# Performance work log

Measured on AMD Instinct MI355X. Metric: run time of the kernel, lower is better.

The kernel has to match this reference:

```python
import jax, jax.numpy as jnp
from jax import lax
import numpy as np


def setup_inputs() -> dict:
    key = jax.random.key(0)
    k1, k2 = jax.random.split(key)
    inputs = jax.random.normal(k1, (32, 64, 64, 128), dtype=jnp.float32)
    # glorot-like scale for a 3x3x128->256 kernel
    kernel = jax.random.normal(k2, (3, 3, 128, 256), dtype=jnp.float32) * 0.03
    return {"inputs": inputs, "kernel": kernel}


def reference(inputs, kernel):
    # Stride-1 VALID conv, NHWC inputs, HWIO kernel (same math as the unrolled
    # per-pixel patch*kernel + reduce_sum loop in conv2d_manual).
    conv = lax.conv_general_dilated(
        inputs, kernel,
        window_strides=(1, 1), padding="VALID",
        dimension_numbers=("NHWC", "HWIO", "NHWC"),
    )  # [B, OH, OW, F]
    B, OH, OW, F = conv.shape
    # Faithfully replicate the original TensorArray stack (OH*OW, B, F)
    # followed by a raw reshape to (B, OH, OW, F) (element-permuting).
    stacked = jnp.moveaxis(conv, 0, 2)            # (OH, OW, B, F)
    out = stacked.reshape(B, OH, OW, F)           # raw reshape, as in original
    return jax.nn.relu(out)
```

## Files before the change

kernel.cpp:

```cpp
#include <hip/hip_runtime.h>

typedef short bf16x8 __attribute__((ext_vector_type(8)));
typedef float f32x4 __attribute__((ext_vector_type(4)));
typedef unsigned short u16;

__device__ __forceinline__ u16 f2bf(float f) {
    unsigned u = __builtin_bit_cast(unsigned, f);
    u += 0x7FFF + ((u >> 16) & 1);
    return (u16)(u >> 16);
}

constexpr int Hh = 64, Ww = 64, Ci = 128;
constexpr int Fo = 256, OH = 62, OW = 62;
constexpr int Ktot = 3 * 3 * Ci;
constexpr int BM = 128, BK = 64;
constexpr int NSTEP = Ktot / BK;
constexpr int NWG = 1922;
constexpr long NEL_IN = 32L * 64 * 64 * 128;
constexpr size_t WS_IN_BYTES = (size_t)NEL_IN * 2;
constexpr size_t WS_WT_OFF   = WS_IN_BYTES;
constexpr size_t WS_NEED     = WS_IN_BYTES + 294912ull * 2;

#define GLD_LDS(src, dst) __builtin_amdgcn_global_load_lds( \
    (const __attribute__((address_space(1))) unsigned int*)(src), \
    (__attribute__((address_space(3))) unsigned int*)(dst), 16, 0, 0)

__global__ __launch_bounds__(256) void cvt_input(const float* __restrict__ in,
                                                 u16* __restrict__ ob) {
    const int i = blockIdx.x * 256 + threadIdx.x;
    const float4* s = (const float4*)in + (long)i * 2;
    float4 v0 = s[0], v1 = s[1];
    bf16x8 p;
    p[0] = (short)f2bf(v0.x); p[1] = (short)f2bf(v0.y);
    p[2] = (short)f2bf(v0.z); p[3] = (short)f2bf(v0.w);
    p[4] = (short)f2bf(v1.x); p[5] = (short)f2bf(v1.y);
    p[6] = (short)f2bf(v1.z); p[7] = (short)f2bf(v1.w);
    ((bf16x8*)ob)[i] = p;
}

__global__ __launch_bounds__(256) void cvt_wt(const float* __restrict__ wt,
                                              u16* __restrict__ ob) {
    const int t = blockIdx.x * 256 + threadIdx.x;
    const int f = t / 144, k8 = t % 144;
    bf16x8 p;
    #pragma unroll
    for (int j = 0; j < 8; ++j)
        p[j] = (short)f2bf(wt[(k8 * 8 + j) * Fo + f]);
    ((bf16x8*)ob)[f * 144 + k8] = p;
}

__global__ __launch_bounds__(256) void conv_mfma(
    const u16* __restrict__ inb,
    const u16* __restrict__ wtb,
    float* __restrict__ out)
{
    __shared__ __align__(16) short As0[BM * BK];
    __shared__ __align__(16) short Bs0[BM * BK];
    __shared__ __align__(16) short As1[BM * BK];
    __shared__ __align__(16) short Bs1[BM * BK];

    const int tid  = threadIdx.x;
    const int lane = tid & 63;
    const int wv   = tid >> 6;
    const int wr   = wv >> 1, wc = wv & 1;

    constexpr int q = NWG / 8, rr = NWG % 8;
    const int orig = blockIdx.x;
    const int xcd = orig & 7, idx = orig >> 3;
    const int wgid = (xcd < rr ? xcd * (q + 1) : rr * (q + 1) + (xcd - rr) * q) + idx;

    const int colb = wgid & 1;
    const int rowb = wgid >> 1;
    const int r0   = rowb * BM;
    const int f0g  = colb * 128;

    const int lrow8 = lane >> 3;
    const int schunk = ((lane & 7) ^ lrow8) * 16;
    long abyte[4], bbyte[4];
    #pragma unroll
    for (int j = 0; j < 4; ++j) {
        const int r  = r0 + wv * 32 + j * 8 + lrow8;
        const int bb = r & 31;
        const int pix = r >> 5;
        const int ow = pix % OW, oh = pix / OW;
        abyte[j] = (long)(((bb * Hh + oh) * Ww + ow) * Ci) * 2 + schunk;
        const int f = f0g + wv * 32 + j * 8 + lrow8;
        bbyte[j] = (long)f * (Ktot * 2) + schunk;
    }

    auto stage = [&](int step, short (&Asb)[BM * BK], short (&Bsb)[BM * BK]) {
        const int kb = step >> 1, c0 = (step & 1) << 6;
        const int kh = kb / 3, kw = kb % 3;
        const long tap = (long)((kh * Ww + kw) * Ci + c0) * 2;
        const long bof = (long)step * 128;
        #pragma unroll
        for (int j = 0; j < 4; ++j)
            GLD_LDS((const char*)inb + abyte[j] + tap, &Asb[(wv * 32 + j * 8) * BK]);
        #pragma unroll
        for (int j = 0; j < 4; ++j)
            GLD_LDS((const char*)wtb + bbyte[j] + bof, &Bsb[(wv * 32 + j * 8) * BK]);
    };

    f32x4 acc[4][4];
    #pragma unroll
    for (int m = 0; m < 4; ++m)
        #pragma unroll
        for (int n = 0; n < 4; ++n) acc[m][n] = (f32x4){0.f, 0.f, 0.f, 0.f};

    const int lrow = lane & 15;
    const int lq   = lane >> 4;

    auto compute = [&](const short (&Asb)[BM * BK], const short (&Bsb)[BM * BK]) {
        #pragma unroll
        for (int ks = 0; ks < 2; ++ks) {
            bf16x8 a[4], b[4];
            const int off = ks * 64 + lq * 16;
            #pragma unroll
            for (int m = 0; m < 4; ++m) {
                const int row = wr * 64 + m * 16 + lrow;
                a[m] = *(const bf16x8*)((const char*)&Asb[0] + row * 128 + (off ^ ((row & 7) << 4)));
            }
            #pragma unroll
            for (int n = 0; n < 4; ++n) {
                const int row = wc * 64 + n * 16 + lrow;
                b[n] = *(const bf16x8*)((const char*)&Bsb[0] + row * 128 + (off ^ ((row & 7) << 4)));
            }
            #pragma unroll
            for (int m = 0; m < 4; ++m)
                #pragma unroll
                for (int n = 0; n < 4; ++n)
                    acc[m][n] = __builtin_amdgcn_mfma_f32_16x16x32_bf16(a[m], b[n], acc[m][n], 0, 0, 0);
        }
    };

    stage(0, As0, Bs0);
    __syncthreads();

    for (int t = 0; t < NSTEP; t += 2) {
        stage(t + 1, As1, Bs1);
        compute(As0, Bs0);
        __syncthreads();
        if (t + 2 < NSTEP) stage(t + 2, As0, Bs0);
        compute(As1, Bs1);
        __syncthreads();
    }

    const int lcol = lane & 15;
    const int lr4  = (lane >> 4) * 4;
    #pragma unroll
    for (int m = 0; m < 4; ++m) {
        #pragma unroll
        for (int n = 0; n < 4; ++n) {
            const int col = f0g + wc * 64 + n * 16 + lcol;
            const int rowbase = r0 + wr * 64 + m * 16 + lr4;
            #pragma unroll
            for (int e = 0; e < 4; ++e) {
                float v = acc[m][n][e];
                out[(long)(rowbase + e) * Fo + col] = v > 0.f ? v : 0.f;
            }
        }
    }
}

__global__ __launch_bounds__(256) void conv_mfma_fb(
    const float* __restrict__ in, const float* __restrict__ wt,
    float* __restrict__ out)
{
    __shared__ __align__(16) short As[BM * BK];
    __shared__ __align__(16) short Bs[BM * BK];
    const int tid  = threadIdx.x;
    const int lane = tid & 63;
    const int wv   = tid >> 6;
    const int wr   = wv >> 1, wc = wv & 1;
    constexpr int q2 = NWG / 8, rr2 = NWG % 8;
    const int orig = blockIdx.x;
    const int xcd = orig & 7, idx = orig >> 3;
    const int wgid = (xcd < rr2 ? xcd * (q2 + 1) : rr2 * (q2 + 1) + (xcd - rr2) * q2) + idx;
    const int colb = wgid & 1;
    const int rowb = wgid >> 1;
    const int r0   = rowb * 128;
    const int f0g  = colb * 128;
    const int ai = tid >> 1;
    const int ah = tid & 1;
    const int r  = r0 + ai;
    const int bb  = r & 31;
    const int pix = r >> 5;
    const int ow  = pix % OW;
    const int oh  = pix / OW;
    const float* abase = in + ((bb * Hh + oh) * Ww + ow) * Ci;
    const int bk = tid & 63;
    const int bf = (tid >> 6) * 32;

    auto loadA = [&](int step, float4 (&pa)[8]) {
        const int kb = step >> 1;
        const int c0 = (step & 1) << 6;
        const int kh = kb / 3, kw = kb % 3;
        const float* src = abase + (kh * Ww + kw) * Ci + c0 + ah * 32;
        #pragma unroll
        for (int c = 0; c < 8; ++c) pa[c] = ((const float4*)src)[c];
    };
    auto writeA = [&](const float4 (&pa)[8]) {
        char* dst = (char*)As + ai * 128;
        const int swz = (ai & 7) << 4;
        #pragma unroll
        for (int c = 0; c < 4; ++c) {
            float4 v0 = pa[2 * c], v1 = pa[2 * c + 1];
            bf16x8 pk;
            pk[0] = (short)f2bf(v0.x); pk[1] = (short)f2bf(v0.y);
            pk[2] = (short)f2bf(v0.z); pk[3] = (short)f2bf(v0.w);
            pk[4] = (short)f2bf(v1.x); pk[5] = (short)f2bf(v1.y);
            pk[6] = (short)f2bf(v1.z); pk[7] = (short)f2bf(v1.w);
            *(bf16x8*)(dst + ((ah * 64 + c * 16) ^ swz)) = pk;
        }
    };
    auto loadB = [&](int step, float4 (&pb)[8]) {
        const float* src = wt + (step * BK + bk) * Fo + f0g + bf;
        #pragma unroll
        for (int c = 0; c < 8; ++c) pb[c] = ((const float4*)src)[c];
    };
    auto writeB = [&](const float4 (&pb)[8]) {
        const int k2 = bk * 2;
        #pragma unroll
        for (int c = 0; c < 8; ++c) {
            float4 v = pb[c];
            const int fl = bf + c * 4;
            *(u16*)((char*)Bs + (fl + 0) * 128 + (k2 ^ (((fl + 0) & 7) << 4))) = f2bf(v.x);
            *(u16*)((char*)Bs + (fl + 1) * 128 + (k2 ^ (((fl + 1) & 7) << 4))) = f2bf(v.y);
            *(u16*)((char*)Bs + (fl + 2) * 128 + (k2 ^ (((fl + 2) & 7) << 4))) = f2bf(v.z);
            *(u16*)((char*)Bs + (fl + 3) * 128 + (k2 ^ (((fl + 3) & 7) << 4))) = f2bf(v.w);
        }
    };

    f32x4 acc[4][4];
    #pragma unroll
    for (int m = 0; m < 4; ++m)
        #pragma unroll
        for (int n = 0; n < 4; ++n) acc[m][n] = (f32x4){0.f, 0.f, 0.f, 0.f};
    {
        float4 pa[8], pb[8];
        loadA(0, pa); loadB(0, pb);
        writeA(pa); writeB(pb);
    }
    __syncthreads();
    const int lrow = lane & 15;
    const int lq   = lane >> 4;
    for (int step = 0; step < NSTEP; ++step) {
        float4 na[8], nb[8];
        if (step + 1 < NSTEP) { loadA(step + 1, na); loadB(step + 1, nb); }
        #pragma unroll
        for (int ks = 0; ks < 2; ++ks) {
            bf16x8 a[4], b[4];
            const int off = ks * 64 + lq * 16;
            #pragma unroll
            for (int m = 0; m < 4; ++m) {
                const int row = wr * 64 + m * 16 + lrow;
                a[m] = *(const bf16x8*)((const char*)As + row * 128 + (off ^ ((row & 7) << 4)));
            }
            #pragma unroll
            for (int n = 0; n < 4; ++n) {
                const int row = wc * 64 + n * 16 + lrow;
                b[n] = *(const bf16x8*)((const char*)Bs + row * 128 + (off ^ ((row & 7) << 4)));
            }
            #pragma unroll
            for (int m = 0; m < 4; ++m)
                #pragma unroll
                for (int n = 0; n < 4; ++n)
                    acc[m][n] = __builtin_amdgcn_mfma_f32_16x16x32_bf16(a[m], b[n], acc[m][n], 0, 0, 0);
        }
        __syncthreads();
        if (step + 1 < NSTEP) { writeA(na); writeB(nb); }
        __syncthreads();
    }
    const int lcol = lane & 15;
    const int lr4  = (lane >> 4) * 4;
    #pragma unroll
    for (int m = 0; m < 4; ++m) {
        #pragma unroll
        for (int n = 0; n < 4; ++n) {
            const int col = f0g + wc * 64 + n * 16 + lcol;
            const int rowbase = r0 + wr * 64 + m * 16 + lr4;
            #pragma unroll
            for (int e = 0; e < 4; ++e) {
                float v = acc[m][n][e];
                out[(rowbase + e) * Fo + col] = v > 0.f ? v : 0.f;
            }
        }
    }
}

extern "C" void kernel_launch(void* const* d_in, const int* in_sizes, int n_in,
                              void* d_out, int out_size, void* d_ws, size_t ws_size,
                              hipStream_t stream) {
    const float* in  = (const float*)d_in[0];
    const float* wt  = (const float*)d_in[1];
    float* out = (float*)d_out;
    if (ws_size >= WS_NEED) {
        u16* inb = (u16*)d_ws;
        u16* wtb = (u16*)((char*)d_ws + WS_WT_OFF);
        cvt_input<<<dim3(8192), dim3(256), 0, stream>>>(in, inb);
        cvt_wt<<<dim3(144), dim3(256), 0, stream>>>(wt, wtb);
        conv_mfma<<<dim3(NWG), dim3(256), 0, stream>>>(inb, wtb, out);
    } else {
        conv_mfma_fb<<<dim3(NWG), dim3(256), 0, stream>>>(in, wt, out);
    }
}
```

Before: 107.0 us.

## Enlarge conv tile to 256x256 with 8 waves and deeper prefetch

The MFMA conv kernel now gives each workgroup a 256-row by all-256-filter output tile with 512 threads (8 waves, each computing 128x64), so 481 workgroups replace 1922. Loads are issued two stages ahead, and synchronisation uses explicit vmcnt waits with raw barriers, with setprio raised around the MFMA bursts. The aim is more reuse per LDS load, fewer redundant input reads, and overlap of global-to-LDS copies with compute. The costs are higher register pressure from 32 accumulators per wave, lower occupancy, a tail workgroup that needs row clamping and guarded stores, and uneven load across the 256 CUs with only 481 groups.

```diff
diff --git a/kernel.cpp b/kernel.cpp
--- a/kernel.cpp
+++ b/kernel.cpp
@@ -13,9 +13,10 @@
 constexpr int Hh = 64, Ww = 64, Ci = 128;
 constexpr int Fo = 256, OH = 62, OW = 62;
 constexpr int Ktot = 3 * 3 * Ci;
-constexpr int BM = 128, BK = 64;
+constexpr int M_TOT = 123008;
+constexpr int BM = 256, BK = 64;
 constexpr int NSTEP = Ktot / BK;
-constexpr int NWG = 1922;
+constexpr int NWG = 481;
 constexpr long NEL_IN = 32L * 64 * 64 * 128;
 constexpr size_t WS_IN_BYTES = (size_t)NEL_IN * 2;
 constexpr size_t WS_WT_OFF   = WS_IN_BYTES;
@@ -24,6 +25,7 @@
 #define GLD_LDS(src, dst) __builtin_amdgcn_global_load_lds( \
     (const __attribute__((address_space(1))) unsigned int*)(src), \
     (__attribute__((address_space(3))) unsigned int*)(dst), 16, 0, 0)
+#define MEMFENCE asm volatile("" ::: "memory")
 
 __global__ __launch_bounds__(256) void cvt_input(const float* __restrict__ in,
                                                  u16* __restrict__ ob) {
@@ -49,7 +51,7 @@
     ((bf16x8*)ob)[f * 144 + k8] = p;
 }
 
-__global__ __launch_bounds__(256) void conv_mfma(
+__global__ __launch_bounds__(512) void conv_mfma(
     const u16* __restrict__ inb,
     const u16* __restrict__ wtb,
     float* __restrict__ out)
@@ -62,29 +64,26 @@
     const int tid  = threadIdx.x;
     const int lane = tid & 63;
     const int wv   = tid >> 6;
-    const int wr   = wv >> 1, wc = wv & 1;
+    const int wr   = wv >> 2, wc = wv & 3;
 
     constexpr int q = NWG / 8, rr = NWG % 8;
     const int orig = blockIdx.x;
     const int xcd = orig & 7, idx = orig >> 3;
     const int wgid = (xcd < rr ? xcd * (q + 1) : rr * (q + 1) + (xcd - rr) * q) + idx;
-
-    const int colb = wgid & 1;
-    const int rowb = wgid >> 1;
-    const int r0   = rowb * BM;
-    const int f0g  = colb * 128;
+    const int r0 = wgid * BM;
 
     const int lrow8 = lane >> 3;
     const int schunk = ((lane & 7) ^ lrow8) * 16;
     long abyte[4], bbyte[4];
     #pragma unroll
     for (int j = 0; j < 4; ++j) {
-        const int r  = r0 + wv * 32 + j * 8 + lrow8;
+        int r = r0 + wv * 32 + j * 8 + lrow8;
+        r = r < M_TOT ? r : M_TOT - 1;
         const int bb = r & 31;
         const int pix = r >> 5;
         const int ow = pix % OW, oh = pix / OW;
         abyte[j] = (long)(((bb * Hh + oh) * Ww + ow) * Ci) * 2 + schunk;
-        const int f = f0g + wv * 32 + j * 8 + lrow8;
+        const int f = wv * 32 + j * 8 + lrow8;
         bbyte[j] = (long)f * (Ktot * 2) + schunk;
     }
 
@@ -101,9 +100,9 @@
             GLD_LDS((const char*)wtb + bbyte[j] + bof, &Bsb[(wv * 32 + j * 8) * BK]);
     };
 
-    f32x4 acc[4][4];
-    #pragma unroll
-    for (int m = 0; m < 4; ++m)
+    f32x4 acc[8][4];
+    #pragma unroll
+    for (int m = 0; m < 8; ++m)
         #pragma unroll
         for (int n = 0; n < 4; ++n) acc[m][n] = (f32x4){0.f, 0.f, 0.f, 0.f};
 
@@ -113,50 +112,91 @@
     auto compute = [&](const short (&Asb)[BM * BK], const short (&Bsb)[BM * BK]) {
         #pragma unroll
         for (int ks = 0; ks < 2; ++ks) {
-            bf16x8 a[4], b[4];
+            bf16x8 a[8], b[4];
             const int off = ks * 64 + lq * 16;
             #pragma unroll
-            for (int m = 0; m < 4; ++m) {
-                const int row = wr * 64 + m * 16 + lrow;
+            for (int m = 0; m < 8; ++m) {
+                const int row = wr * 128 + m * 16 + lrow;
                 a[m] = *(const bf16x8*)((const char*)&Asb[0] + row * 128 + (off ^ ((row & 7) << 4)));
             }
             #pragma unroll
             for (int n = 0; n < 4; ++n) {
-                const int row = wc * 64 + n * 16 + lrow;
-                b[n] = *(const bf16x8*)((const char*)&Bsb[0] + row * 128 + (off ^ ((row & 7) << 4)));
-            }
-            #pragma unroll
-            for (int m = 0; m < 4; ++m)
+                const int frow = wc * 64 + n * 16 + lrow;
+                b[n] = *(const bf16x8*)((const char*)&Bsb[0] + frow * 128 + (off ^ ((frow & 7) << 4)));
+            }
+            __builtin_amdgcn_s_setprio(1);
+            #pragma unroll
+            for (int m = 0; m < 8; ++m)
                 #pragma unroll
                 for (int n = 0; n < 4; ++n)
                     acc[m][n] = __builtin_amdgcn_mfma_f32_16x16x32_bf16(a[m], b[n], acc[m][n], 0, 0, 0);
+            __builtin_amdgcn_s_setprio(0);
         }
     };
 
     stage(0, As0, Bs0);
-    __syncthreads();
+    stage(1, As1, Bs1);
+    asm volatile("s_waitcnt vmcnt(8)" ::: "memory");
+    __builtin_amdgcn_s_barrier();
+    MEMFENCE;
 
     for (int t = 0; t < NSTEP; t += 2) {
-        stage(t + 1, As1, Bs1);
         compute(As0, Bs0);
-        __syncthreads();
-        if (t + 2 < NSTEP) stage(t + 2, As0, Bs0);
+        MEMFENCE;
+        __builtin_amdgcn_s_barrier();
+        MEMFENCE;
+        if (t + 2 < NSTEP) {
+            stage(t + 2, As0, Bs0);
+            asm volatile("s_waitcnt vmcnt(8)" ::: "memory");
+        } else {
+            asm volatile("s_waitcnt vmcnt(0)" ::: "memory");
+        }
+        __builtin_amdgcn_s_barrier();
+        MEMFENCE;
+
         compute(As1, Bs1);
-        __syncthreads();
+        MEMFENCE;
+        __builtin_amdgcn_s_barrier();
+        MEMFENCE;
+        if (t + 3 < NSTEP) {
+            stage(t + 3, As1, Bs1);
+            asm volatile("s_waitcnt vmcnt(8)" ::: "memory");
+        } else {
+            asm volatile("s_waitcnt vmcnt(0)" ::: "memory");
+        }
+        __builtin_amdgcn_s_barrier();
+        MEMFENCE;
     }
 
     const int lcol = lane & 15;
     const int lr4  = (lane >> 4) * 4;
-    #pragma unroll
-    for (int m = 0; m < 4; ++m) {
-        #pragma unroll
-        for (int n = 0; n < 4; ++n) {
-            const int col = f0g + wc * 64 + n * 16 + lcol;
-            const int rowbase = r0 + wr * 64 + m * 16 + lr4;
-            #pragma unroll
-            for (int e = 0; e < 4; ++e) {
-                float v = acc[m][n][e];
-                out[(long)(rowbase + e) * Fo + col] = v > 0.f ? v : 0.f;
+    const int col  = wc * 64 + lcol;
+    if (r0 + BM <= M_TOT) {
+        #pragma unroll
+        for (int m = 0; m < 8; ++m) {
+            const int rowbase = r0 + wr * 128 + m * 16 + lr4;
+            #pragma unroll
+            for (int n = 0; n < 4; ++n) {
+                #pragma unroll
+                for (int e = 0; e < 4; ++e) {
+                    float v = acc[m][n][e];
+                    out[(long)(rowbase + e) * Fo + col + n * 16] = v > 0.f ? v : 0.f;
+                }
+            }
+        }
+    } else {
+        #pragma unroll
+        for (int m = 0; m < 8; ++m) {
+            const int rowbase = r0 + wr * 128 + m * 16 + lr4;
+            #pragma unroll
+            for (int n = 0; n < 4; ++n) {
+                #pragma unroll
+                for (int e = 0; e < 4; ++e) {
+                    if (rowbase + e < M_TOT) {
+                        float v = acc[m][n][e];
+                        out[(long)(rowbase + e) * Fo + col + n * 16] = v > 0.f ? v : 0.f;
+                    }
+                }
             }
         }
     }
@@ -166,13 +206,15 @@
     const float* __restrict__ in, const float* __restrict__ wt,
     float* __restrict__ out)
 {
-    __shared__ __align__(16) short As[BM * BK];
-    __shared__ __align__(16) short Bs[BM * BK];
+    constexpr int FBM = 128;
+    __shared__ __align__(16) short As[FBM * BK];
+    __shared__ __align__(16) short Bs[FBM * BK];
     const int tid  = threadIdx.x;
     const int lane = tid & 63;
     const int wv   = tid >> 6;
     const int wr   = wv >> 1, wc = wv & 1;
-    constexpr int q2 = NWG / 8, rr2 = NWG % 8;
+    constexpr int NWG_FB = 1922;
+    constexpr int q2 = NWG_FB / 8, rr2 = NWG_FB % 8;
     const int orig = blockIdx.x;
     const int xcd = orig & 7, idx = orig >> 3;
     const int wgid = (xcd < rr2 ? xcd * (q2 + 1) : rr2 * (q2 + 1) + (xcd - rr2) * q2) + idx;
@@ -227,7 +269,7 @@
             *(u16*)((char*)Bs + (fl + 0) * 128 + (k2 ^ (((fl + 0) & 7) << 4))) = f2bf(v.x);
             *(u16*)((char*)Bs + (fl + 1) * 128 + (k2 ^ (((fl + 1) & 7) << 4))) = f2bf(v.y);
             *(u16*)((char*)Bs + (fl + 2) * 128 + (k2 ^ (((fl + 2) & 7) << 4))) = f2bf(v.z);
-            *(u16*)((char*)Bs + (fl + 3) * 128 + (k2 ^ (((fl + 3) & 7) << 4))) = f2bf(v.w);
+            *(u16*)((char*)Bs + (fl + 3) * 128 + (k2 ^ (((fl + 3) << 4) & 0x70))) = f2bf(v.w);
         }
     };
 
@@ -299,8 +341,8 @@
         u16* wtb = (u16*)((char*)d_ws + WS_WT_OFF);
         cvt_input<<<dim3(8192), dim3(256), 0, stream>>>(in, inb);
         cvt_wt<<<dim3(144), dim3(256), 0, stream>>>(wt, wtb);
-        conv_mfma<<<dim3(NWG), dim3(256), 0, stream>>>(inb, wtb, out);
+        conv_mfma<<<dim3(NWG), dim3(512), 0, stream>>>(inb, wtb, out);
     } else {
-        conv_mfma_fb<<<dim3(NWG), dim3(256), 0, stream>>>(in, wt, out);
-    }
-}
+        conv_mfma_fb<<<dim3(1922), dim3(256), 0, stream>>>(in, wt, out);
+    }
+}
```

After: 107.0 us. No clear change (+0.0%).

## Load weight fragments directly from global into registers, dropping B LDS staging

Applied to the files above, without the earlier changes.

Weights are pre-permuted at conversion time into an MFMA-fragment-ordered layout, so each lane can read its B operands straight from global memory into registers, double-buffered across steps. The B shared-memory buffers and their LDS reads are removed, halving LDS use and LDS traffic. The cost is more VGPRs for two sets of eight bf16x8 fragments and direct global loads that depend on L2 hits for the shared weight tile, which may lower occupancy or expose load latency.

```diff
diff --git a/kernel.cpp b/kernel.cpp
--- a/kernel.cpp
+++ b/kernel.cpp
@@ -41,12 +41,14 @@
 __global__ __launch_bounds__(256) void cvt_wt(const float* __restrict__ wt,
                                               u16* __restrict__ ob) {
     const int t = blockIdx.x * 256 + threadIdx.x;
-    const int f = t / 144, k8 = t % 144;
+    const int lq  = t & 3;
+    const int f   = (t >> 2) & 255;
+    const int sks = t >> 10;
     bf16x8 p;
     #pragma unroll
     for (int j = 0; j < 8; ++j)
-        p[j] = (short)f2bf(wt[(k8 * 8 + j) * Fo + f]);
-    ((bf16x8*)ob)[f * 144 + k8] = p;
+        p[j] = (short)f2bf(wt[(sks * 32 + lq * 8 + j) * Fo + f]);
+    ((bf16x8*)ob)[t] = p;
 }
 
 __global__ __launch_bounds__(256) void conv_mfma(
@@ -55,9 +57,7 @@
     float* __restrict__ out)
 {
     __shared__ __align__(16) short As0[BM * BK];
-    __shared__ __align__(16) short Bs0[BM * BK];
     __shared__ __align__(16) short As1[BM * BK];
-    __shared__ __align__(16) short Bs1[BM * BK];
 
     const int tid  = threadIdx.x;
     const int lane = tid & 63;
@@ -72,11 +72,10 @@
     const int colb = wgid & 1;
     const int rowb = wgid >> 1;
     const int r0   = rowb * BM;
-    const int f0g  = colb * 128;
 
     const int lrow8 = lane >> 3;
     const int schunk = ((lane & 7) ^ lrow8) * 16;
-    long abyte[4], bbyte[4];
+    long abyte[4];
     #pragma unroll
     for (int j = 0; j < 4; ++j) {
         const int r  = r0 + wv * 32 + j * 8 + lrow8;
@@ -84,36 +83,40 @@
         const int pix = r >> 5;
         const int ow = pix % OW, oh = pix / OW;
         abyte[j] = (long)(((bb * Hh + oh) * Ww + ow) * Ci) * 2 + schunk;
-        const int f = f0g + wv * 32 + j * 8 + lrow8;
-        bbyte[j] = (long)f * (Ktot * 2) + schunk;
-    }
-
-    auto stage = [&](int step, short (&Asb)[BM * BK], short (&Bsb)[BM * BK]) {
+    }
+
+    auto stage = [&](int step, short (&Asb)[BM * BK]) {
         const int kb = step >> 1, c0 = (step & 1) << 6;
         const int kh = kb / 3, kw = kb % 3;
         const long tap = (long)((kh * Ww + kw) * Ci + c0) * 2;
-        const long bof = (long)step * 128;
         #pragma unroll
         for (int j = 0; j < 4; ++j)
             GLD_LDS((const char*)inb + abyte[j] + tap, &Asb[(wv * 32 + j * 8) * BK]);
-        #pragma unroll
-        for (int j = 0; j < 4; ++j)
-            GLD_LDS((const char*)wtb + bbyte[j] + bof, &Bsb[(wv * 32 + j * 8) * BK]);
-    };
-
-    f32x4 acc[4][4];
-    #pragma unroll
-    for (int m = 0; m < 4; ++m)
-        #pragma unroll
-        for (int n = 0; n < 4; ++n) acc[m][n] = (f32x4){0.f, 0.f, 0.f, 0.f};
+    };
 
     const int lrow = lane & 15;
     const int lq   = lane >> 4;
 
-    auto compute = [&](const short (&Asb)[BM * BK], const short (&Bsb)[BM * BK]) {
+    const bf16x8* bsrc = (const bf16x8*)wtb;
+    const int bbase = (colb * 128 + wc * 64 + lrow) * 4 + lq;
+    auto loadB = [&](int step, bf16x8 (&bf)[8]) {
+        #pragma unroll
+        for (int ks = 0; ks < 2; ++ks)
+            #pragma unroll
+            for (int n = 0; n < 4; ++n)
+                bf[ks * 4 + n] = bsrc[(step * 2 + ks) * 1024 + bbase + n * 64];
+    };
+
+    f32x4 acc[4][4];
+    #pragma unroll
+    for (int m = 0; m < 4; ++m)
+        #pragma unroll
+        for (int n = 0; n < 4; ++n) acc[m][n] = (f32x4){0.f, 0.f, 0.f, 0.f};
+
+    auto compute = [&](const short (&Asb)[BM * BK], const bf16x8 (&bfr)[8]) {
         #pragma unroll
         for (int ks = 0; ks < 2; ++ks) {
-            bf16x8 a[4], b[4];
+            bf16x8 a[4];
             const int off = ks * 64 + lq * 16;
             #pragma unroll
             for (int m = 0; m < 4; ++m) {
@@ -121,27 +124,29 @@
                 a[m] = *(const bf16x8*)((const char*)&Asb[0] + row * 128 + (off ^ ((row & 7) << 4)));
             }
             #pragma unroll
-            for (int n = 0; n < 4; ++n) {
-                const int row = wc * 64 + n * 16 + lrow;
-                b[n] = *(const bf16x8*)((const char*)&Bsb[0] + row * 128 + (off ^ ((row & 7) << 4)));
-            }
-            #pragma unroll
             for (int m = 0; m < 4; ++m)
                 #pragma unroll
                 for (int n = 0; n < 4; ++n)
-                    acc[m][n] = __builtin_amdgcn_mfma_f32_16x16x32_bf16(a[m], b[n], acc[m][n], 0, 0, 0);
-        }
-    };
-
-    stage(0, As0, Bs0);
+                    acc[m][n] = __builtin_amdgcn_mfma_f32_16x16x32_bf16(a[m], bfr[ks * 4 + n], acc[m][n], 0, 0, 0);
+        }
+    };
+
+    bf16x8 b0[8], b1[8];
+
+    stage(0, As0);
+    loadB(0, b0);
     __syncthreads();
 
     for (int t = 0; t < NSTEP; t += 2) {
-        stage(t + 1, As1, Bs1);
-        compute(As0, Bs0);
+        stage(t + 1, As1);
+        loadB(t + 1, b1);
+        compute(As0, b0);
         __syncthreads();
-        if (t + 2 < NSTEP) stage(t + 2, As0, Bs0);
-        compute(As1, Bs1);
+        if (t + 2 < NSTEP) {
+            stage(t + 2, As0);
+            loadB(t + 2, b0);
+        }
+        compute(As1, b1);
         __syncthreads();
     }
 
@@ -151,7 +156,7 @@
     for (int m = 0; m < 4; ++m) {
         #pragma unroll
         for (int n = 0; n < 4; ++n) {
-            const int col = f0g + wc * 64 + n * 16 + lcol;
+            const int col = colb * 128 + wc * 64 + n * 16 + lcol;
             const int rowbase = r0 + wr * 64 + m * 16 + lr4;
             #pragma unroll
             for (int e = 0; e < 4; ++e) {
```

Measured after the change: 132.5 us. 23.9% more time.

## Widen K tile to a full tap, single-buffer LDS, and merge conversion kernels

Applied to the files above, without the earlier changes.

The main conv kernel now loads a full 3x3 tap (128 channels) per step, so there are 9 K-steps instead of 18. The double-buffered LDS pair is replaced by a single 32 KB A/B buffer with a 16-way XOR swizzle, and the next stage is issued after the compute barrier. The two bf16 conversion kernels are merged into one launch. This halves the number of barriers and removes a launch, but global-to-LDS loads no longer overlap with MFMA compute inside a workgroup. The design instead relies on multiple resident workgroups per CU to hide load latency.

```diff
diff --git a/kernel.cpp b/kernel.cpp
--- a/kernel.cpp
+++ b/kernel.cpp
@@ -13,8 +13,8 @@
 constexpr int Hh = 64, Ww = 64, Ci = 128;
 constexpr int Fo = 256, OH = 62, OW = 62;
 constexpr int Ktot = 3 * 3 * Ci;
-constexpr int BM = 128, BK = 64;
-constexpr int NSTEP = Ktot / BK;
+constexpr int BM = 128, BK = 128;
+constexpr int NSTEP = 9;
 constexpr int NWG = 1922;
 constexpr long NEL_IN = 32L * 64 * 64 * 128;
 constexpr size_t WS_IN_BYTES = (size_t)NEL_IN * 2;
@@ -25,28 +25,30 @@
     (const __attribute__((address_space(1))) unsigned int*)(src), \
     (__attribute__((address_space(3))) unsigned int*)(dst), 16, 0, 0)
 
-__global__ __launch_bounds__(256) void cvt_input(const float* __restrict__ in,
-                                                 u16* __restrict__ ob) {
-    const int i = blockIdx.x * 256 + threadIdx.x;
-    const float4* s = (const float4*)in + (long)i * 2;
-    float4 v0 = s[0], v1 = s[1];
-    bf16x8 p;
-    p[0] = (short)f2bf(v0.x); p[1] = (short)f2bf(v0.y);
-    p[2] = (short)f2bf(v0.z); p[3] = (short)f2bf(v0.w);
-    p[4] = (short)f2bf(v1.x); p[5] = (short)f2bf(v1.y);
-    p[6] = (short)f2bf(v1.z); p[7] = (short)f2bf(v1.w);
-    ((bf16x8*)ob)[i] = p;
-}
-
-__global__ __launch_bounds__(256) void cvt_wt(const float* __restrict__ wt,
-                                              u16* __restrict__ ob) {
-    const int t = blockIdx.x * 256 + threadIdx.x;
-    const int f = t / 144, k8 = t % 144;
-    bf16x8 p;
-    #pragma unroll
-    for (int j = 0; j < 8; ++j)
-        p[j] = (short)f2bf(wt[(k8 * 8 + j) * Fo + f]);
-    ((bf16x8*)ob)[f * 144 + k8] = p;
+__global__ __launch_bounds__(256) void cvt_all(const float* __restrict__ in,
+                                               const float* __restrict__ wt,
+                                               u16* __restrict__ inb,
+                                               u16* __restrict__ wtb) {
+    const int b = blockIdx.x;
+    if (b < 8192) {
+        const int i = b * 256 + threadIdx.x;
+        const float4* s = (const float4*)in + (long)i * 2;
+        float4 v0 = s[0], v1 = s[1];
+        bf16x8 p;
+        p[0] = (short)f2bf(v0.x); p[1] = (short)f2bf(v0.y);
+        p[2] = (short)f2bf(v0.z); p[3] = (short)f2bf(v0.w);
+        p[4] = (short)f2bf(v1.x); p[5] = (short)f2bf(v1.y);
+        p[6] = (short)f2bf(v1.z); p[7] = (short)f2bf(v1.w);
+        ((bf16x8*)inb)[i] = p;
+    } else {
+        const int t = (b - 8192) * 256 + threadIdx.x;
+        const int f = t / 144, k8 = t % 144;
+        bf16x8 p;
+        #pragma unroll
+        for (int j = 0; j < 8; ++j)
+            p[j] = (short)f2bf(wt[(k8 * 8 + j) * Fo + f]);
+        ((bf16x8*)wtb)[f * 144 + k8] = p;
+    }
 }
 
 __global__ __launch_bounds__(256) void conv_mfma(
@@ -54,10 +56,8 @@
     const u16* __restrict__ wtb,
     float* __restrict__ out)
 {
-    __shared__ __align__(16) short As0[BM * BK];
-    __shared__ __align__(16) short Bs0[BM * BK];
-    __shared__ __align__(16) short As1[BM * BK];
-    __shared__ __align__(16) short Bs1[BM * BK];
+    __shared__ __align__(16) short As[BM * BK];
+    __shared__ __align__(16) short Bs[BM * BK];
 
     const int tid  = threadIdx.x;
     const int lane = tid & 63;
@@ -74,31 +74,31 @@
     const int r0   = rowb * BM;
     const int f0g  = colb * 128;
 
-    const int lrow8 = lane >> 3;
-    const int schunk = ((lane & 7) ^ lrow8) * 16;
-    long abyte[4], bbyte[4];
-    #pragma unroll
-    for (int j = 0; j < 4; ++j) {
-        const int r  = r0 + wv * 32 + j * 8 + lrow8;
+    const int lrow4 = lane >> 4;
+    const int chunk = lane & 15;
+    int abyte[8], bbyte[8];
+    #pragma unroll
+    for (int j = 0; j < 8; ++j) {
+        const int rl = wv * 32 + j * 4 + lrow4;
+        const int sw = (chunk ^ (rl & 15)) * 16;
+        const int r  = r0 + rl;
         const int bb = r & 31;
         const int pix = r >> 5;
         const int ow = pix % OW, oh = pix / OW;
-        abyte[j] = (long)(((bb * Hh + oh) * Ww + ow) * Ci) * 2 + schunk;
-        const int f = f0g + wv * 32 + j * 8 + lrow8;
-        bbyte[j] = (long)f * (Ktot * 2) + schunk;
-    }
-
-    auto stage = [&](int step, short (&Asb)[BM * BK], short (&Bsb)[BM * BK]) {
-        const int kb = step >> 1, c0 = (step & 1) << 6;
-        const int kh = kb / 3, kw = kb % 3;
-        const long tap = (long)((kh * Ww + kw) * Ci + c0) * 2;
-        const long bof = (long)step * 128;
-        #pragma unroll
-        for (int j = 0; j < 4; ++j)
-            GLD_LDS((const char*)inb + abyte[j] + tap, &Asb[(wv * 32 + j * 8) * BK]);
-        #pragma unroll
-        for (int j = 0; j < 4; ++j)
-            GLD_LDS((const char*)wtb + bbyte[j] + bof, &Bsb[(wv * 32 + j * 8) * BK]);
+        abyte[j] = ((bb * Hh + oh) * Ww + ow) * Ci * 2 + sw;
+        bbyte[j] = (f0g + rl) * (Ktot * 2) + sw;
+    }
+
+    auto stage = [&](int step) {
+        const int kh = step / 3, kw = step % 3;
+        const int tap = (kh * Ww + kw) * Ci * 2;
+        const int bof = step * 256;
+        #pragma unroll
+        for (int j = 0; j < 8; ++j)
+            GLD_LDS((const char*)inb + abyte[j] + tap, &As[(wv * 32 + j * 4) * BK]);
+        #pragma unroll
+        for (int j = 0; j < 8; ++j)
+            GLD_LDS((const char*)wtb + bbyte[j] + bof, &Bs[(wv * 32 + j * 4) * BK]);
     };
 
     f32x4 acc[4][4];
@@ -106,24 +106,27 @@
     for (int m = 0; m < 4; ++m)
         #pragma unroll
         for (int n = 0; n < 4; ++n) acc[m][n] = (f32x4){0.f, 0.f, 0.f, 0.f};
+
+    stage(0);
 
     const int lrow = lane & 15;
     const int lq   = lane >> 4;
 
-    auto compute = [&](const short (&Asb)[BM * BK], const short (&Bsb)[BM * BK]) {
-        #pragma unroll
-        for (int ks = 0; ks < 2; ++ks) {
+    for (int step = 0; step < NSTEP; ++step) {
+        __syncthreads();
+        #pragma unroll
+        for (int ks = 0; ks < 4; ++ks) {
             bf16x8 a[4], b[4];
             const int off = ks * 64 + lq * 16;
             #pragma unroll
             for (int m = 0; m < 4; ++m) {
                 const int row = wr * 64 + m * 16 + lrow;
-                a[m] = *(const bf16x8*)((const char*)&Asb[0] + row * 128 + (off ^ ((row & 7) << 4)));
+                a[m] = *(const bf16x8*)((const char*)As + row * 256 + (off ^ ((row & 15) << 4)));
             }
             #pragma unroll
             for (int n = 0; n < 4; ++n) {
-                const int row = wc * 64 + n * 16 + lrow;
-                b[n] = *(const bf16x8*)((const char*)&Bsb[0] + row * 128 + (off ^ ((row & 7) << 4)));
+                const int frow = wc * 64 + n * 16 + lrow;
+                b[n] = *(const bf16x8*)((const char*)Bs + frow * 256 + (off ^ ((frow & 15) << 4)));
             }
             #pragma unroll
             for (int m = 0; m < 4; ++m)
@@ -131,18 +134,8 @@
                 for (int n = 0; n < 4; ++n)
                     acc[m][n] = __builtin_amdgcn_mfma_f32_16x16x32_bf16(a[m], b[n], acc[m][n], 0, 0, 0);
         }
-    };
-
-    stage(0, As0, Bs0);
-    __syncthreads();
-
-    for (int t = 0; t < NSTEP; t += 2) {
-        stage(t + 1, As1, Bs1);
-        compute(As0, Bs0);
-        __syncthreads();
-        if (t + 2 < NSTEP) stage(t + 2, As0, Bs0);
-        compute(As1, Bs1);
-        __syncthreads();
+        __syncthreads();
+        if (step + 1 < NSTEP) stage(step + 1);
     }
 
     const int lcol = lane & 15;
@@ -166,8 +159,8 @@
     const float* __restrict__ in, const float* __restrict__ wt,
     float* __restrict__ out)
 {
-    __shared__ __align__(16) short As[BM * BK];
-    __shared__ __align__(16) short Bs[BM * BK];
+    __shared__ __align__(16) short As[128 * 64];
+    __shared__ __align__(16) short Bs[128 * 64];
     const int tid  = threadIdx.x;
     const int lane = tid & 63;
     const int wv   = tid >> 6;
@@ -190,6 +183,7 @@
     const float* abase = in + ((bb * Hh + oh) * Ww + ow) * Ci;
     const int bk = tid & 63;
     const int bf = (tid >> 6) * 32;
+    constexpr int FNSTEP = 18;
 
     auto loadA = [&](int step, float4 (&pa)[8]) {
         const int kb = step >> 1;
@@ -214,7 +208,7 @@
         }
     };
     auto loadB = [&](int step, float4 (&pb)[8]) {
-        const float* src = wt + (step * BK + bk) * Fo + f0g + bf;
+        const float* src = wt + (step * 64 + bk) * Fo + f0g + bf;
         #pragma unroll
         for (int c = 0; c < 8; ++c) pb[c] = ((const float4*)src)[c];
     };
@@ -244,9 +238,9 @@
     __syncthreads();
     const int lrow = lane & 15;
     const int lq   = lane >> 4;
-    for (int step = 0; step < NSTEP; ++step) {
+    for (int step = 0; step < FNSTEP; ++step) {
         float4 na[8], nb[8];
-        if (step + 1 < NSTEP) { loadA(step + 1, na); loadB(step + 1, nb); }
+        if (step + 1 < FNSTEP) { loadA(step + 1, na); loadB(step + 1, nb); }
         #pragma unroll
         for (int ks = 0; ks < 2; ++ks) {
             bf16x8 a[4], b[4];
@@ -268,7 +262,7 @@
                     acc[m][n] = __builtin_amdgcn_mfma_f32_16x16x32_bf16(a[m], b[n], acc[m][n], 0, 0, 0);
         }
         __syncthreads();
-        if (step + 1 < NSTEP) { writeA(na); writeB(nb); }
+        if (step + 1 < FNSTEP) { writeA(na); writeB(nb); }
         __syncthreads();
     }
     const int lcol = lane & 15;
@@ -297,8 +291,7 @@
     if (ws_size >= WS_NEED) {
         u16* inb = (u16*)d_ws;
         u16* wtb = (u16*)((char*)d_ws + WS_WT_OFF);
-        cvt_input<<<dim3(8192), dim3(256), 0, stream>>>(in, inb);
-        cvt_wt<<<dim3(144), dim3(256), 0, stream>>>(wt, wtb);
+        cvt_all<<<dim3(8336), dim3(256), 0, stream>>>(in, wt, inb, wtb);
         conv_mfma<<<dim3(NWG), dim3(256), 0, stream>>>(inb, wtb, out);
     } else {
         conv_mfma_fb<<<dim3(NWG), dim3(256), 0, stream>>>(in, wt, out);
```

Measured after the change: 98.39 us. -8.0%, faster.
